# Kernel optimization log

Measured on AMD Instinct MI355X. Metric: run time of the kernel, lower is better.

## Reference

```python
import jax, jax.numpy as jnp
import numpy as np

VQ_ALPHA = 0.5   # non-trainable vq_alpha weight, constant 0.5
BETA = 0.25      # commitment loss weight


def setup_inputs() -> dict:
    key = jax.random.key(0)
    k1, k2 = jax.random.split(key)
    x = jax.random.normal(k1, (16, 64, 64, 256), dtype=jnp.float32)
    # tf.keras RandomUniform default is U(-0.05, 0.05)
    dictionary = jax.random.uniform(k2, (256, 1024), dtype=jnp.float32,
                                    minval=-0.05, maxval=0.05)
    return {"x": x, "dictionary": dictionary}


def reference(x, dictionary):
    D, K = dictionary.shape  # embedding_dim, num_embeddings
    flat = x.reshape(-1, D)  # [N, D]

    # squared L2 distances: ||f||^2 + ||d||^2 - 2 f.d   -> [N, K]
    similarity = flat @ dictionary
    distances = (jnp.sum(flat * flat, axis=1, keepdims=True)
                 + jnp.sum(dictionary * dictionary, axis=0, keepdims=True)
                 - 2.0 * similarity)
    code_idx = jnp.argmin(distances, axis=1)  # [N]

    # one-hot @ dict^T is just a row gather of dict^T
    quantized = jnp.take(dictionary.T, code_idx, axis=0)  # [N, D]
    quantized = VQ_ALPHA * quantized
    q = quantized.reshape(x.shape)

    dictionary_loss = jnp.mean(jnp.square(jax.lax.stop_gradient(x) - q))
    commitment_loss = jnp.mean(jnp.square(x - jax.lax.stop_gradient(q)))
    loss = dictionary_loss + BETA * commitment_loss

    # straight-through estimator
    q_st = x + jax.lax.stop_gradient(q - x)
    return q_st, loss
```

## Files before the change

kernel.cpp:

```cpp
#include <hip/hip_runtime.h>


#define NROWS   65536
#define DIM     256
#define NCODE   1024
#define RPB     64
#define NBLK    (NROWS / RPB)
#define EPS_TIE 6e-3f

typedef _Float16 half8 __attribute__((ext_vector_type(8)));
typedef float    f32x4 __attribute__((ext_vector_type(4)));

__global__ void k_prep(const float* __restrict__ dict, float* __restrict__ dictT,
                       float* __restrict__ dictnorm, unsigned short* __restrict__ packB) {
    int gid = blockIdx.x * 256 + threadIdx.x;
#pragma unroll
    for (int ii = 0; ii < 4; ++ii) {
        int e = ii * 65536 + gid;
        { int d = e >> 10, k = e & 1023; dictT[k * DIM + d] = dict[e]; }
        { int j = e & 7, o = (e >> 3) & 2047, cc = e >> 14;
          int l15 = o & 15, q = (o >> 4) & 3, t = (o >> 6) & 3, kk = o >> 8;
          int d = kk * 32 + q * 8 + j;
          int n = cc * 64 + t * 16 + l15;
          _Float16 h = (_Float16)dict[d * NCODE + n];
          packB[e] = *(unsigned short*)&h; }
    }
    if (blockIdx.x < 4) {
        int k = blockIdx.x * 256 + threadIdx.x;
        float s = 0.f;
#pragma unroll 8
        for (int d = 0; d < DIM; ++d) {
            float v = dict[d * NCODE + k];
            s = fmaf(v, v, s);
        }
        dictnorm[k] = s + 8.0f;
    }
}

__device__ __forceinline__ float np_pairwise_sq_128(const float* a, int stride) {
    float r[8];
#pragma unroll
    for (int j = 0; j < 8; ++j) {
        float v = a[j * stride];
        r[j] = __fmul_rn(v, v);
    }
    for (int i = 8; i < 128; i += 8) {
#pragma unroll
        for (int j = 0; j < 8; ++j) {
            float v = a[(i + j) * stride];
            r[j] = __fadd_rn(r[j], __fmul_rn(v, v));
        }
    }
    return __fadd_rn(__fadd_rn(__fadd_rn(r[0], r[1]), __fadd_rn(r[2], r[3])),
                     __fadd_rn(__fadd_rn(r[4], r[5]), __fadd_rn(r[6], r[7])));
}


__global__ __launch_bounds__(256, 4) void k_vq(
    const float* __restrict__ x, const float* __restrict__ dict,
    const float* __restrict__ dictT, const float* __restrict__ dictnorm,
    const unsigned short* __restrict__ packB,
    float* __restrict__ out, double* __restrict__ block_sums)
{
    __shared__ __align__(16) unsigned short bstage[16384];
    __shared__ float row_gap[RPB];
    __shared__ int   row_k1[RPB];
    __shared__ float red_d[256];
    __shared__ int   red_k[256];
    __shared__ float wred[4];
    __shared__ int   amb_list[RPB];
    __shared__ int   amb_cnt;

    const int tid  = threadIdx.x;
    const int ln   = tid & 63, wv = tid >> 6;
    const int l15  = ln & 15, q = ln >> 4;
    const int row0 = blockIdx.x * RPB;

    if (tid == 0) amb_cnt = 0;

    half8 afrag[8];
    {
        const float* ar = x + (size_t)(row0 + wv * 16 + l15) * DIM + q * 8;
#pragma unroll
        for (int kk = 0; kk < 8; ++kk) {
            const float4 p0 = *(const float4*)(ar + kk * 32);
            const float4 p1 = *(const float4*)(ar + kk * 32 + 4);
            half8 h;
            h[0] = (_Float16)p0.x; h[1] = (_Float16)p0.y; h[2] = (_Float16)p0.z; h[3] = (_Float16)p0.w;
            h[4] = (_Float16)p1.x; h[5] = (_Float16)p1.y; h[6] = (_Float16)p1.z; h[7] = (_Float16)p1.w;
            afrag[kk] = h;
        }
    }

    unsigned p1v[4], p2v[4];
#pragma unroll
    for (int i = 0; i < 4; ++i) { p1v[i] = 0xFFFFFFFFu; p2v[i] = 0xFFFFFFFFu; }

    for (int cc = 0; cc < 16; ++cc) {
        const int c0 = cc * 64;
        __syncthreads();
        {
            const unsigned short* src = packB + (size_t)cc * 16384 + tid * 8;
            uint4 tmp[8];
#pragma unroll
            for (int p = 0; p < 8; ++p) tmp[p] = *(const uint4*)(src + p * 2048);
#pragma unroll
            for (int p = 0; p < 8; ++p) *(uint4*)&bstage[p * 2048 + tid * 8] = tmp[p];
        }
        __syncthreads();

        float dn[4];
#pragma unroll
        for (int t = 0; t < 4; ++t) dn[t] = dictnorm[c0 + t * 16 + l15];

        const f32x4 zero = {0.f, 0.f, 0.f, 0.f};
        f32x4 acc[4];
#pragma unroll
        for (int t = 0; t < 4; ++t) acc[t] = zero;

#pragma unroll
        for (int kk = 0; kk < 8; ++kk) {
#pragma unroll
            for (int t = 0; t < 4; ++t) {
                const half8 b = *(const half8*)&bstage[(kk * 4 + t) * 512 + q * 128 + l15 * 8];
                acc[t] = __builtin_amdgcn_mfma_f32_16x16x32_f16(afrag[kk], b, acc[t], 0, 0, 0);
            }
        }

#pragma unroll
        for (int t = 0; t < 4; ++t) {
            const unsigned kbase = (unsigned)(c0 + t * 16 + l15);
#pragma unroll
            for (int i = 0; i < 4; ++i) {
                const float s = fmaf(-2.f, acc[t][i], dn[t]);
                const unsigned pk = (__float_as_uint(s) & 0xFFFFFC00u) | kbase;
                const unsigned mx = p1v[i] > pk ? p1v[i] : pk;
                p2v[i] = p2v[i] < mx ? p2v[i] : mx;
                p1v[i] = p1v[i] < pk ? p1v[i] : pk;
            }
        }
    }

#pragma unroll
    for (int i = 0; i < 4; ++i) {
        unsigned a1 = p1v[i], a2 = p2v[i];
#pragma unroll
        for (int m = 1; m < 16; m <<= 1) {
            const unsigned o1 = __shfl_xor(a1, m);
            const unsigned o2 = __shfl_xor(a2, m);
            const unsigned mx = a1 > o1 ? a1 : o1;
            a1 = a1 < o1 ? a1 : o1;
            const unsigned mn2 = a2 < o2 ? a2 : o2;
            a2 = mx < mn2 ? mx : mn2;
        }
        if (l15 == 0) {
            const int r = wv * 16 + q * 4 + i;
            row_k1[r]  = (int)(a1 & 1023u);
            row_gap[r] = __uint_as_float(a2 & 0xFFFFFC00u) - __uint_as_float(a1 & 0xFFFFFC00u);
        }
    }
    __syncthreads();

    if (tid < RPB && row_gap[tid] < EPS_TIE) {
        int p = atomicAdd(&amb_cnt, 1);
        amb_list[p] = tid;
    }
    __syncthreads();
    const int namb = amb_cnt;

    for (int a = 0; a < namb; ++a) {
        const int r = amb_list[a];
        const float* xr = x + (size_t)(row0 + r) * DIM;
        const float nf = __fadd_rn(np_pairwise_sq_128(xr, 1), np_pairwise_sq_128(xr + 128, 1));
        float bd = 3.4e38f; int bk = 0x7fffffff;
#pragma unroll
        for (int i = 0; i < 4; ++i) {
            const int k = i * 256 + tid;
            float sim = 0.f, nd = 0.f;
            for (int d = 0; d < DIM; ++d) {
                const float dv = dict[(size_t)d * NCODE + k];
                const float fv = xr[d];
                sim = fmaf(fv, dv, sim);
                nd  = __fadd_rn(nd, __fmul_rn(dv, dv));
            }
            const float dist = __fsub_rn(__fadd_rn(nf, nd), __fmul_rn(2.f, sim));
            if (dist < bd) { bd = dist; bk = k; }
        }
        red_d[tid] = bd; red_k[tid] = bk;
        __syncthreads();
        for (int s = 128; s > 0; s >>= 1) {
            if (tid < s) {
                const float od = red_d[tid + s]; const int ok = red_k[tid + s];
                if (od < red_d[tid] || (od == red_d[tid] && ok < red_k[tid])) {
                    red_d[tid] = od; red_k[tid] = ok;
                }
            }
            __syncthreads();
        }
        if (tid == 0) row_k1[r] = red_k[0];
        __syncthreads();
    }

    float lsum = 0.f;
#pragma unroll 2
    for (int i = 0; i < 16; ++i) {
        const int e = i * 1024 + tid * 4;
        const int r = e >> 8, d0 = e & 255;
        const int kk = row_k1[r];
        const float4 dv = *(const float4*)&dictT[(size_t)kk * DIM + d0];
        const float4 xv = *(const float4*)&x[(size_t)row0 * DIM + e];
        float4 qv; qv.x = 0.5f * dv.x; qv.y = 0.5f * dv.y; qv.z = 0.5f * dv.z; qv.w = 0.5f * dv.w;
        float4 ov;
        ov.x = __fadd_rn(xv.x, __fsub_rn(qv.x, xv.x));
        ov.y = __fadd_rn(xv.y, __fsub_rn(qv.y, xv.y));
        ov.z = __fadd_rn(xv.z, __fsub_rn(qv.z, xv.z));
        ov.w = __fadd_rn(xv.w, __fsub_rn(qv.w, xv.w));
        const float e0 = __fsub_rn(xv.x, qv.x), e1 = __fsub_rn(xv.y, qv.y);
        const float e2 = __fsub_rn(xv.z, qv.z), e3 = __fsub_rn(xv.w, qv.w);
        lsum += e0 * e0 + e1 * e1 + e2 * e2 + e3 * e3;
        *(float4*)&out[(size_t)row0 * DIM + e] = ov;
    }

#pragma unroll
    for (int sft = 32; sft > 0; sft >>= 1) lsum += __shfl_down(lsum, sft, 64);
    if ((tid & 63) == 0) wred[tid >> 6] = lsum;
    __syncthreads();
    if (tid == 0)
        block_sums[blockIdx.x] = (double)((wred[0] + wred[1]) + (wred[2] + wred[3]));
}


__global__ void k_finalize(const double* __restrict__ block_sums, float* __restrict__ out_loss) {
    __shared__ double w[16];
    const int t = threadIdx.x;
    double v = block_sums[t];
#pragma unroll
    for (int sft = 32; sft > 0; sft >>= 1) v += __shfl_down(v, sft, 64);
    if ((t & 63) == 0) w[t >> 6] = v;
    __syncthreads();
    if (t == 0) {
        double tot = 0.0;
        for (int i = 0; i < 16; ++i) tot += w[i];
        out_loss[0] = (float)(1.25 * tot / (double)(NROWS * DIM));
    }
}


extern "C" void kernel_launch(void* const* d_in, const int* in_sizes, int n_in,
                              void* d_out, int out_size, void* d_ws, size_t ws_size,
                              hipStream_t stream) {
    (void)in_sizes; (void)n_in; (void)out_size; (void)ws_size;
    const float* x    = (const float*)d_in[0];
    const float* dict = (const float*)d_in[1];
    float* out = (float*)d_out;

    char* ws = (char*)d_ws;
    float*          dictT      = (float*)ws;
    float*          dictnorm   = (float*)(ws + 1048576);
    double*         block_sums = (double*)(ws + 1048576 + 4096);
    unsigned short* packB      = (unsigned short*)(ws + 1048576 + 4096 + 8192);

    k_prep<<<256, 256, 0, stream>>>(dict, dictT, dictnorm, packB);
    k_vq<<<NBLK, 256, 0, stream>>>(x, dict, dictT, dictnorm, packB, out, block_sums);
    k_finalize<<<1, 1024, 0, stream>>>(block_sums, out + (size_t)NROWS * DIM);
}
```

Before: 324.9 us.

## Double-buffer codebook staging with direct global-to-LDS loads and smaller chunks

The codebook tile is now double-buffered in shared memory, so the next 32-code chunk is fetched while the current one feeds the MFMAs. The fetch uses global_load_lds, which writes straight into LDS without passing through registers. The packed-fp16 layout in the prep kernel is rearranged for 32-code chunks and written from a coalesced read of dict. Chunk size is halved to keep the shared-memory footprint unchanged, which doubles the number of iterations and barriers and gives less MFMA work per chunk to hide load latency.

```diff
diff --git a/kernel.cpp b/kernel.cpp
--- a/kernel.cpp
+++ b/kernel.cpp
@@ -6,6 +6,7 @@
 #define NCODE   1024
 #define RPB     64
 #define NBLK    (NROWS / RPB)
+#define NCHUNK  32
 #define EPS_TIE 6e-3f
 
 typedef _Float16 half8 __attribute__((ext_vector_type(8)));
@@ -17,13 +18,13 @@
 #pragma unroll
     for (int ii = 0; ii < 4; ++ii) {
         int e = ii * 65536 + gid;
-        { int d = e >> 10, k = e & 1023; dictT[k * DIM + d] = dict[e]; }
-        { int j = e & 7, o = (e >> 3) & 2047, cc = e >> 14;
-          int l15 = o & 15, q = (o >> 4) & 3, t = (o >> 6) & 3, kk = o >> 8;
-          int d = kk * 32 + q * 8 + j;
-          int n = cc * 64 + t * 16 + l15;
-          _Float16 h = (_Float16)dict[d * NCODE + n];
-          packB[e] = *(unsigned short*)&h; }
+        const float v = dict[e];
+        const int d = e >> 10, k = e & 1023;
+        dictT[k * DIM + d] = v;
+        _Float16 h = (_Float16)v;
+        const int o = (k >> 5) * 8192 + ((d >> 5) * 2 + ((k >> 4) & 1)) * 512
+                    + ((d >> 3) & 3) * 128 + (k & 15) * 8 + (d & 7);
+        packB[o] = *(unsigned short*)&h;
     }
     if (blockIdx.x < 4) {
         int k = blockIdx.x * 256 + threadIdx.x;
@@ -56,13 +57,24 @@
 }
 
 
+#define STAGE(buf, cc) do {                                                            \
+    const unsigned short* _s = packB + (size_t)(cc) * 8192 + tid * 8;                  \
+    unsigned short* _d = &bstage[buf][tid * 8];                                        \
+    _Pragma("unroll")                                                                  \
+    for (int _p = 0; _p < 4; ++_p)                                                     \
+        __builtin_amdgcn_global_load_lds(                                              \
+            (const __attribute__((address_space(1))) unsigned int*)(_s + _p * 2048),   \
+            (__attribute__((address_space(3))) unsigned int*)(_d + _p * 2048),         \
+            16, 0, 0);                                                                 \
+} while (0)
+
 __global__ __launch_bounds__(256, 4) void k_vq(
     const float* __restrict__ x, const float* __restrict__ dict,
     const float* __restrict__ dictT, const float* __restrict__ dictnorm,
     const unsigned short* __restrict__ packB,
     float* __restrict__ out, double* __restrict__ block_sums)
 {
-    __shared__ __align__(16) unsigned short bstage[16384];
+    __shared__ __align__(16) unsigned short bstage[2][8192];
     __shared__ float row_gap[RPB];
     __shared__ int   row_k1[RPB];
     __shared__ float red_d[256];
@@ -76,6 +88,7 @@
     const int l15  = ln & 15, q = ln >> 4;
     const int row0 = blockIdx.x * RPB;
 
+    STAGE(0, 0);
     if (tid == 0) amb_cnt = 0;
 
     half8 afrag[8];
@@ -96,39 +109,31 @@
 #pragma unroll
     for (int i = 0; i < 4; ++i) { p1v[i] = 0xFFFFFFFFu; p2v[i] = 0xFFFFFFFFu; }
 
-    for (int cc = 0; cc < 16; ++cc) {
-        const int c0 = cc * 64;
-        __syncthreads();
-        {
-            const unsigned short* src = packB + (size_t)cc * 16384 + tid * 8;
-            uint4 tmp[8];
-#pragma unroll
-            for (int p = 0; p < 8; ++p) tmp[p] = *(const uint4*)(src + p * 2048);
-#pragma unroll
-            for (int p = 0; p < 8; ++p) *(uint4*)&bstage[p * 2048 + tid * 8] = tmp[p];
-        }
-        __syncthreads();
-
-        float dn[4];
-#pragma unroll
-        for (int t = 0; t < 4; ++t) dn[t] = dictnorm[c0 + t * 16 + l15];
+    __syncthreads();
+
+    for (int cc = 0; cc < NCHUNK; ++cc) {
+        const int cur = cc & 1;
+        if (cc < NCHUNK - 1) STAGE(cur ^ 1, cc + 1);
+        const int c0 = cc * 32;
+        float dn[2];
+#pragma unroll
+        for (int t = 0; t < 2; ++t) dn[t] = dictnorm[c0 + t * 16 + l15];
 
         const f32x4 zero = {0.f, 0.f, 0.f, 0.f};
-        f32x4 acc[4];
-#pragma unroll
-        for (int t = 0; t < 4; ++t) acc[t] = zero;
+        f32x4 acc[2];
+        acc[0] = zero; acc[1] = zero;
 
 #pragma unroll
         for (int kk = 0; kk < 8; ++kk) {
 #pragma unroll
-            for (int t = 0; t < 4; ++t) {
-                const half8 b = *(const half8*)&bstage[(kk * 4 + t) * 512 + q * 128 + l15 * 8];
+            for (int t = 0; t < 2; ++t) {
+                const half8 b = *(const half8*)&bstage[cur][(kk * 2 + t) * 512 + q * 128 + l15 * 8];
                 acc[t] = __builtin_amdgcn_mfma_f32_16x16x32_f16(afrag[kk], b, acc[t], 0, 0, 0);
             }
         }
 
 #pragma unroll
-        for (int t = 0; t < 4; ++t) {
+        for (int t = 0; t < 2; ++t) {
             const unsigned kbase = (unsigned)(c0 + t * 16 + l15);
 #pragma unroll
             for (int i = 0; i < 4; ++i) {
@@ -139,6 +144,7 @@
                 p1v[i] = p1v[i] < pk ? p1v[i] : pk;
             }
         }
+        __syncthreads();
     }
 
 #pragma unroll
```

Result: slower. 335.0 us (+3.1%).
